# Kernel optimization log

Measured on AMD Instinct MI355X. Metric: run time of the kernel, lower is better.

Reference implementation:

```python
import jax, jax.numpy as jnp
import numpy as np

N = 100000
E = 1600000
G = 64  # number of graphs
EPS = 1e-5
NEG_SLOPE = 0.2


def _gat_conv(x, W, a_src, a_dst, b, src, dst, n, H, C):
    # x: [n, in]; W: [in, H*C]; a_src/a_dst: [H, C]; b: [H*C]
    h = (x @ W).reshape(n, H, C)                      # [n,H,C]
    al_s = jnp.sum(h * a_src, axis=-1)                # [n,H]
    al_d = jnp.sum(h * a_dst, axis=-1)                # [n,H]
    score = jax.nn.leaky_relu(al_s[src] + al_d[dst], NEG_SLOPE)  # [E,H]
    # segment softmax over incoming edges of each dst node
    m = jax.ops.segment_max(score, dst, num_segments=n)
    ex = jnp.exp(score - jax.lax.stop_gradient(m)[dst])
    den = jax.ops.segment_sum(ex, dst, num_segments=n)
    alpha = ex / den[dst]                             # [E,H]
    out = jax.ops.segment_sum(alpha[:, :, None] * h[src], dst, num_segments=n)
    return out.reshape(n, H * C) + b


def _bn_relu(x, gamma, beta):
    mu = jnp.mean(x, axis=0)
    var = jnp.var(x, axis=0)  # biased, matches torch BN normalization
    return jax.nn.relu((x - mu) * jax.lax.rsqrt(var + EPS) * gamma + beta)


def setup_inputs() -> dict:
    key = jax.random.key(0)
    ks = jax.random.split(key, 32)
    d = {}
    d['x'] = jax.random.normal(ks[0], (N, 3), dtype=jnp.float32)
    d['edge_index'] = jax.random.randint(ks[1], (2, E), 0, N, dtype=jnp.int64)
    d['batch'] = jnp.sort(jax.random.randint(ks[2], (N,), 0, G, dtype=jnp.int64))
    def p(k, shape):
        return jax.random.normal(k, shape, dtype=jnp.float32) * 0.1
    # conv1: 3 -> 16, heads=2
    d['W1'] = p(ks[3], (3, 32)); d['as1'] = p(ks[4], (2, 16)); d['ad1'] = p(ks[5], (2, 16)); d['b1'] = p(ks[6], (32,))
    d['g1'] = jnp.ones((32,), jnp.float32); d['be1'] = jnp.zeros((32,), jnp.float32)
    # conv2: 32 -> 32, heads=2
    d['W2'] = p(ks[7], (32, 64)); d['as2'] = p(ks[8], (2, 32)); d['ad2'] = p(ks[9], (2, 32)); d['b2'] = p(ks[10], (64,))
    d['g2'] = jnp.ones((64,), jnp.float32); d['be2'] = jnp.zeros((64,), jnp.float32)
    # conv3: 64 -> 64, heads=2
    d['W3'] = p(ks[11], (64, 128)); d['as3'] = p(ks[12], (2, 64)); d['ad3'] = p(ks[13], (2, 64)); d['b3'] = p(ks[14], (128,))
    d['g3'] = jnp.ones((128,), jnp.float32); d['be3'] = jnp.zeros((128,), jnp.float32)
    d['fcw'] = p(ks[15], (128, 10)); d['fcb'] = p(ks[16], (10,))
    return d


def reference(x, edge_index, batch, W1, as1, ad1, b1, g1, be1, W2, as2, ad2, b2, g2, be2, W3, as3, ad3, b3, g3, be3, fcw, fcb):
    n = x.shape[0]
    loops = jnp.arange(n, dtype=edge_index.dtype)  # PyG GATConv add_self_loops=True
    src = jnp.concatenate([edge_index[0], loops])
    dst = jnp.concatenate([edge_index[1], loops])
    h = _bn_relu(_gat_conv(x, W1, as1, ad1, b1, src, dst, n, 2, 16), g1, be1)
    h = _bn_relu(_gat_conv(h, W2, as2, ad2, b2, src, dst, n, 2, 32), g2, be2)
    h = _bn_relu(_gat_conv(h, W3, as3, ad3, b3, src, dst, n, 2, 64), g3, be3)
    pooled = jax.ops.segment_max(h, batch, num_segments=G)  # [G,128]
    return pooled @ fcw + fcb
```

## Files before the change

### kernel.cpp

```cpp
#include <hip/hip_runtime.h>
#include <cstddef>

constexpr int NN = 100000;
constexpr int NE = 1600000;
constexpr int TE = NE + NN;
constexpr int NG = 64;
constexpr float EPS = 1e-5f;
constexpr float NEG_SLOPE = 0.2f;
constexpr int NREP = 16;

constexpr int NBUCK = 256;
constexpr int DPB = 391;
constexpr int PHB = 256;
constexpr int CH = (TE + PHB - 1) / PHB;

__device__ __forceinline__ unsigned short f2bf(float f) {
    unsigned u = __float_as_uint(f);
    u += 0x7fffu + ((u >> 16) & 1u);
    return (unsigned short)(u >> 16);
}
__device__ __forceinline__ float bf2f(unsigned short s) {
    return __uint_as_float((unsigned)s << 16);
}
__device__ __forceinline__ float bflo(unsigned u) { return __uint_as_float(u << 16); }
__device__ __forceinline__ float bfhi(unsigned u) { return __uint_as_float(u & 0xffff0000u); }


__global__ void k_hist(const int* __restrict__ ei, int* __restrict__ hist) {
    __shared__ int hcnt[NBUCK];
    for (int i = threadIdx.x; i < NBUCK; i += 256) hcnt[i] = 0;
    __syncthreads();
    int k = blockIdx.x;
    int e0 = k * CH, e1 = min(e0 + CH, TE);
    for (int e = e0 + threadIdx.x; e < e1; e += 256) {
        int d = (e < NE) ? ei[NE + e] : (e - NE);
        atomicAdd(&hcnt[d / DPB], 1);
    }
    __syncthreads();
    for (int b = threadIdx.x; b < NBUCK; b += 256) hist[b * PHB + k] = hcnt[b];
}

__global__ void k_scanA(int* __restrict__ hist, int* __restrict__ bsum) {
    __shared__ int ls[PHB];
    int b = blockIdx.x, t = threadIdx.x;
    int v = hist[b * PHB + t];
    ls[t] = v;
    __syncthreads();
    for (int off = 1; off < PHB; off <<= 1) {
        int add = (t >= off) ? ls[t - off] : 0;
        __syncthreads();
        ls[t] += add;
        __syncthreads();
    }
    hist[b * PHB + t] = ls[t] - v;
    if (t == PHB - 1) bsum[b] = ls[t];
}

__global__ void k_scanB(const int* __restrict__ bsum, int* __restrict__ bbase,
                        int* __restrict__ rowptr) {
    __shared__ int ls[NBUCK];
    int t = threadIdx.x;
    int v = bsum[t];
    ls[t] = v;
    __syncthreads();
    for (int off = 1; off < NBUCK; off <<= 1) {
        int add = (t >= off) ? ls[t - off] : 0;
        __syncthreads();
        ls[t] += add;
        __syncthreads();
    }
    bbase[t] = ls[t] - v;
    if (t == NBUCK - 1) { bbase[NBUCK] = ls[t]; rowptr[NN] = ls[t]; }
}

__global__ void k_scatter(const int* __restrict__ ei, const int* __restrict__ hist,
                          const int* __restrict__ bbase, int* __restrict__ pairs) {
    __shared__ int cur[NBUCK];
    int k = blockIdx.x;
    for (int b = threadIdx.x; b < NBUCK; b += 256) cur[b] = bbase[b] + hist[b * PHB + k];
    __syncthreads();
    int e0 = k * CH, e1 = min(e0 + CH, TE);
    for (int e = e0 + threadIdx.x; e < e1; e += 256) {
        int s, d;
        if (e < NE) { s = ei[e]; d = ei[NE + e]; } else { s = e - NE; d = s; }
        int b = d / DPB, ld = d - b * DPB;
        int pos = atomicAdd(&cur[b], 1);
        pairs[pos] = (s << 9) | ld;
    }
}

__global__ void k_csr(const int* __restrict__ pairs, const int* __restrict__ bbase,
                      int* __restrict__ rowptr, int* __restrict__ colsrc) {
    __shared__ int deg[DPB];
    __shared__ int exc[DPB];
    __shared__ int sc[512];
    int b = blockIdx.x, t = threadIdx.x;
    int base = bbase[b], cnt = bbase[b + 1] - base;
    int d0 = b * DPB;
    int ndst = min(DPB, NN - d0);
    for (int i = t; i < DPB; i += 256) deg[i] = 0;
    __syncthreads();
    for (int i = t; i < cnt; i += 256) atomicAdd(&deg[pairs[base + i] & 511], 1);
    __syncthreads();
    sc[t] = (t < DPB) ? deg[t] : 0;
    sc[t + 256] = (t + 256 < DPB) ? deg[t + 256] : 0;
    __syncthreads();
    for (int off = 1; off < 512; off <<= 1) {
        int a0 = (t >= off) ? sc[t - off] : 0;
        int a1 = (t + 256 >= off) ? sc[t + 256 - off] : 0;
        __syncthreads();
        sc[t] += a0; sc[t + 256] += a1;
        __syncthreads();
    }
    if (t < DPB) exc[t] = sc[t] - deg[t];
    if (t + 256 < DPB) exc[t + 256] = sc[t + 256] - deg[t + 256];
    __syncthreads();
    for (int i = t; i < ndst; i += 256) rowptr[d0 + i] = base + exc[i];
    for (int i = t; i < DPB; i += 256) deg[i] = 0;
    __syncthreads();
    for (int i = t; i < cnt; i += 256) {
        int p = pairs[base + i];
        int ld = p & 511;
        int s = (unsigned)p >> 9;
        int pos = base + exc[ld] + atomicAdd(&deg[ld], 1);
        colsrc[pos] = s;
    }
}


template <int IN, int OUT, bool BN, int GRP>
__global__ void k_transform(const void* __restrict__ xv, const float* __restrict__ W,
                            const float* __restrict__ a_src, const float* __restrict__ a_dst,
                            const float* __restrict__ bnrep,
                            const float* __restrict__ gamma, const float* __restrict__ beta,
                            unsigned short* __restrict__ h, float* __restrict__ als,
                            float* __restrict__ ald, int n) {
    constexpr int C = OUT / 2;
    constexpr int TPN = OUT / 4;
    constexpr int NB = 256 / TPN;
    __shared__ float4 Ws4[IN * TPN];
    __shared__ float xs[NB * IN];
    __shared__ float sbn[BN ? 2 * IN : 1];

    if constexpr (BN) {
        if (threadIdx.x < IN) {
            int c = threadIdx.x;
            float s = 0.f, ss = 0.f;
#pragma unroll
            for (int r = 0; r < NREP; ++r) {
                s  += bnrep[r * 2 * IN + c];
                ss += bnrep[r * 2 * IN + IN + c];
            }
            float mu = s / n;
            float var = ss / n - mu * mu;
            float sca = gamma[c] * rsqrtf(var + EPS);
            sbn[c] = sca;
            sbn[IN + c] = beta[c] - mu * sca;
        }
    }
    float* Wsf = (float*)Ws4;
    for (int i = threadIdx.x; i < IN * OUT; i += 256) Wsf[i] = W[i];
    __syncthreads();

    int nl = threadIdx.x / TPN, q = threadIdx.x % TPN;
    int hd = (q >= TPN / 2);
    int cc = (q - hd * (TPN / 2)) * 4;
    float4 as4 = *(const float4*)&a_src[hd * C + cc];
    float4 ad4 = *(const float4*)&a_dst[hd * C + cc];

    for (int g = 0; g < GRP; ++g) {
        int node0 = (blockIdx.x * GRP + g) * NB;
        if (node0 >= n) break;
        if constexpr (BN) {
            const unsigned* xu = (const unsigned*)xv + (size_t)node0 * IN / 2;
            for (int i = threadIdx.x; i < NB * IN / 2; i += 256) {
                int e0 = 2 * i;
                int nn = node0 + e0 / IN;
                unsigned u = (nn < n) ? xu[i] : 0u;
                int c0 = e0 % IN;
                float v0 = bflo(u) * sbn[c0] + sbn[IN + c0];
                float v1 = bfhi(u) * sbn[c0 + 1] + sbn[IN + c0 + 1];
                xs[e0]     = v0 > 0.f ? v0 : 0.f;
                xs[e0 + 1] = v1 > 0.f ? v1 : 0.f;
            }
        } else {
            const float* x = (const float*)xv;
            for (int i = threadIdx.x; i < NB * IN; i += 256) {
                int nn = node0 + i / IN;
                xs[i] = (nn < n) ? x[(size_t)nn * IN + (i % IN)] : 0.f;
            }
        }
        __syncthreads();
        int node = node0 + nl;
        float4 acc = {0.f, 0.f, 0.f, 0.f};
#pragma unroll
        for (int i = 0; i < IN; ++i) {
            float xv2 = xs[nl * IN + i];
            float4 w = Ws4[i * TPN + q];
            acc.x += xv2 * w.x; acc.y += xv2 * w.y; acc.z += xv2 * w.z; acc.w += xv2 * w.w;
        }
        if (node < n) {
            uint2 pk;
            pk.x = (unsigned)f2bf(acc.x) | ((unsigned)f2bf(acc.y) << 16);
            pk.y = (unsigned)f2bf(acc.z) | ((unsigned)f2bf(acc.w) << 16);
            *(uint2*)&h[(size_t)node * OUT + q * 4] = pk;
        }
        float ps = acc.x * as4.x + acc.y * as4.y + acc.z * as4.z + acc.w * as4.w;
        float pd = acc.x * ad4.x + acc.y * ad4.y + acc.z * ad4.z + acc.w * ad4.w;
#pragma unroll
        for (int m = 1; m < TPN / 2; m <<= 1) {
            ps += __shfl_xor(ps, m, 64);
            pd += __shfl_xor(pd, m, 64);
        }
        if ((q & (TPN / 2 - 1)) == 0 && node < n) {
            als[node * 2 + hd] = ps;
            ald[node * 2 + hd] = pd;
        }
        __syncthreads();
    }
}


__device__ __forceinline__ float lrelu(float v) { return v > 0.f ? v : NEG_SLOPE * v; }

template <int OUT>
__global__ void k_aggregate(const int* __restrict__ rowptr, const int* __restrict__ colsrc,
                            const unsigned short* __restrict__ h, const float* __restrict__ als,
                            const float* __restrict__ ald, unsigned short* __restrict__ out,
                            float* __restrict__ bnrep) {
    constexpr int LPE = OUT / 8;
    constexpr int EPI2 = 32 / LPE;
    constexpr int UNR = 4;
    __shared__ float rowbuf[8][OUT];
    __shared__ float4 etab[4][64];
    int wv = threadIdx.x >> 6;
    int lane = threadIdx.x & 63;
    int hw = lane >> 5, hl = lane & 31;
    int base = ((int)blockIdx.x * 4 + wv) * 2;
    int wid = base + hw;
    bool valid = wid < NN;

    int start = 0, cnt = 0;
    float2 dv = make_float2(0.f, 0.f);
    if (valid) {
        start = rowptr[wid];
        cnt = rowptr[wid + 1] - start;
        dv = ((const float2*)ald)[wid];
    }
    int mc = max(cnt, __shfl_xor(cnt, 32, 64));

    if (mc <= 32) {
        int e = start + hl;
        bool act = valid && (hl < cnt);
        int s = act ? colsrc[e] : 0;
        float2 av = act ? ((const float2*)als)[s] : make_float2(0.f, 0.f);
        float t0 = act ? lrelu(av.x + dv.x) : -1e30f;
        float t1 = act ? lrelu(av.y + dv.y) : -1e30f;
        float m0 = t0, m1 = t1;
#pragma unroll
        for (int off = 16; off; off >>= 1) {
            m0 = fmaxf(m0, __shfl_xor(m0, off, 32));
            m1 = fmaxf(m1, __shfl_xor(m1, off, 32));
        }
        float w0 = act ? __expf(t0 - m0) : 0.f;
        float w1 = act ? __expf(t1 - m1) : 0.f;
        float den0 = w0, den1 = w1;
#pragma unroll
        for (int off = 16; off; off >>= 1) {
            den0 += __shfl_xor(den0, off, 32);
            den1 += __shfl_xor(den1, off, 32);
        }
        etab[wv][lane] = make_float4(__int_as_float(s), w0, w1, 0.f);
        int sub = hl / LPE, cl = hl % LPE;
        bool head1 = (cl >= LPE / 2);
        float acc[8];
#pragma unroll
        for (int k = 0; k < 8; ++k) acc[k] = 0.f;
        if (valid) {
            int cm1 = cnt - 1;
            for (int j0 = 0; j0 < cnt; j0 += EPI2 * UNR) {
                float wsl[UNR];
                uint4 hv[UNR];
#pragma unroll
                for (int u = 0; u < UNR; ++u) {
                    int jj = j0 + u * EPI2 + sub;
                    int jc = min(jj, cm1);
                    float4 ed = etab[wv][hw * 32 + jc];
                    wsl[u] = (jj <= cm1) ? (head1 ? ed.z : ed.y) : 0.f;
                    hv[u] = *(const uint4*)&h[(size_t)__float_as_int(ed.x) * OUT + cl * 8];
                }
#pragma unroll
                for (int u = 0; u < UNR; ++u) {
                    float a = wsl[u];
                    acc[0] += a * bflo(hv[u].x); acc[1] += a * bfhi(hv[u].x);
                    acc[2] += a * bflo(hv[u].y); acc[3] += a * bfhi(hv[u].y);
                    acc[4] += a * bflo(hv[u].z); acc[5] += a * bfhi(hv[u].z);
                    acc[6] += a * bflo(hv[u].w); acc[7] += a * bfhi(hv[u].w);
                }
            }
        }
#pragma unroll
        for (int m = LPE; m < 32; m <<= 1) {
#pragma unroll
            for (int k = 0; k < 8; ++k) acc[k] += __shfl_xor(acc[k], m, 32);
        }
        float inv = 1.f / (head1 ? den1 : den0);
        if (valid && sub == 0) {
            float o[8];
#pragma unroll
            for (int k = 0; k < 8; ++k) o[k] = acc[k] * inv;
            uint4 pk;
            pk.x = (unsigned)f2bf(o[0]) | ((unsigned)f2bf(o[1]) << 16);
            pk.y = (unsigned)f2bf(o[2]) | ((unsigned)f2bf(o[3]) << 16);
            pk.z = (unsigned)f2bf(o[4]) | ((unsigned)f2bf(o[5]) << 16);
            pk.w = (unsigned)f2bf(o[6]) | ((unsigned)f2bf(o[7]) << 16);
            *(uint4*)&out[(size_t)wid * OUT + cl * 8] = pk;
            *(float4*)&rowbuf[wv * 2 + hw][cl * 8] = make_float4(o[0], o[1], o[2], o[3]);
            *(float4*)&rowbuf[wv * 2 + hw][cl * 8 + 4] = make_float4(o[4], o[5], o[6], o[7]);
        } else if (!valid) {
            for (int c = hl; c < OUT; c += 32) rowbuf[wv * 2 + hw][c] = 0.f;
        }
    } else {
        for (int i = 0; i < 2; ++i) {
            int w2 = base + i;
            int rb = wv * 2 + i;
            if (w2 >= NN) {
                for (int c = lane; c < OUT; c += 64) rowbuf[rb][c] = 0.f;
                continue;
            }
            int st = rowptr[w2], en = rowptr[w2 + 1];
            float2 dv2 = ((const float2*)ald)[w2];
            constexpr int C = OUT / 2;
            float m0 = -1e30f, m1 = -1e30f;
            for (int e = st + lane; e < en; e += 64) {
                int s = colsrc[e];
                float t0 = lrelu(als[s * 2 + 0] + dv2.x);
                float t1 = lrelu(als[s * 2 + 1] + dv2.y);
                m0 = fmaxf(m0, t0); m1 = fmaxf(m1, t1);
            }
#pragma unroll
            for (int off = 32; off; off >>= 1) {
                m0 = fmaxf(m0, __shfl_xor(m0, off, 64));
                m1 = fmaxf(m1, __shfl_xor(m1, off, 64));
            }
            float den0 = 0.f, den1 = 0.f;
            for (int e = st + lane; e < en; e += 64) {
                int s = colsrc[e];
                float t0 = lrelu(als[s * 2 + 0] + dv2.x);
                float t1 = lrelu(als[s * 2 + 1] + dv2.y);
                den0 += __expf(t0 - m0); den1 += __expf(t1 - m1);
            }
#pragma unroll
            for (int off = 32; off; off >>= 1) {
                den0 += __shfl_xor(den0, off, 64);
                den1 += __shfl_xor(den1, off, 64);
            }
            float inv0 = 1.f / den0, inv1 = 1.f / den1;
            if constexpr (OUT == 128) {
                float a0 = 0.f, a1 = 0.f;
                for (int e = st; e < en; ++e) {
                    int s = colsrc[e];
                    float t0 = lrelu(als[s * 2 + 0] + dv2.x);
                    float t1 = lrelu(als[s * 2 + 1] + dv2.y);
                    float w0 = __expf(t0 - m0) * inv0;
                    float w1 = __expf(t1 - m1) * inv1;
                    a0 += w0 * bf2f(h[(size_t)s * OUT + lane]);
                    a1 += w1 * bf2f(h[(size_t)s * OUT + 64 + lane]);
                }
                out[(size_t)w2 * OUT + lane] = f2bf(a0);
                out[(size_t)w2 * OUT + 64 + lane] = f2bf(a1);
                rowbuf[rb][lane] = a0;
                rowbuf[rb][64 + lane] = a1;
            } else {
                int c = lane;
                bool act2 = c < OUT;
                float a0 = 0.f;
                for (int e = st; e < en; ++e) {
                    int s = colsrc[e];
                    float t0 = lrelu(als[s * 2 + 0] + dv2.x);
                    float t1 = lrelu(als[s * 2 + 1] + dv2.y);
                    float w = (c < C) ? __expf(t0 - m0) * inv0 : __expf(t1 - m1) * inv1;
                    if (act2) a0 += w * bf2f(h[(size_t)s * OUT + c]);
                }
                if (act2) { out[(size_t)w2 * OUT + c] = f2bf(a0); rowbuf[rb][c] = a0; }
            }
        }
    }
    __syncthreads();
    float* dst = &bnrep[(blockIdx.x & (NREP - 1)) * 2 * OUT];
    for (int c = threadIdx.x; c < OUT; c += 256) {
        float s = 0.f, ss = 0.f;
#pragma unroll
        for (int r = 0; r < 8; ++r) {
            float v = rowbuf[r][c];
            s += v; ss += v * v;
        }
        atomicAdd(&dst[c], s);
        atomicAdd(&dst[OUT + c], ss);
    }
}


__global__ void k_pool(const unsigned short* __restrict__ h, const int* __restrict__ batch,
                       const float* __restrict__ bnrep, const float* __restrict__ gamma,
                       const float* __restrict__ beta, float* __restrict__ pooled, int n) {
    const int K = 32;
    int c = threadIdx.x;
    float s = 0.f, ss = 0.f;
#pragma unroll
    for (int r = 0; r < NREP; ++r) {
        s  += bnrep[r * 256 + c];
        ss += bnrep[r * 256 + 128 + c];
    }
    float mu = s / n;
    float var = ss / n - mu * mu;
    float scale = gamma[c] * rsqrtf(var + EPS);
    float shift = beta[c] - mu * scale;
    int n0 = blockIdx.x * K;
    if (n0 >= n) return;
    int nend = min(n, n0 + K);
    int curg = batch[n0];
    float m = 0.f;
    for (int nn = n0; nn < nend; ++nn) {
        int g = batch[nn];
        if (g != curg) {
            atomicMax((int*)&pooled[curg * 128 + c], __float_as_int(m));
            m = 0.f; curg = g;
        }
        float v = bf2f(h[(size_t)nn * 128 + c]) * scale + shift;
        m = fmaxf(m, v > 0.f ? v : 0.f);
    }
    atomicMax((int*)&pooled[curg * 128 + c], __float_as_int(m));
}

__global__ void k_fc(const float* __restrict__ pooled, const float* __restrict__ fcw,
                     const float* __restrict__ fcb, float* __restrict__ out) {
    int t = threadIdx.x;
    if (t >= NG * 10) return;
    int g = t / 10, j = t % 10;
    float acc = fcb[j];
#pragma unroll
    for (int c = 0; c < 128; ++c) acc += pooled[g * 128 + c] * fcw[c * 10 + j];
    out[g * 10 + j] = acc;
}


extern "C" void kernel_launch(void* const* d_in, const int* in_sizes, int n_in,
                              void* d_out, int out_size, void* d_ws, size_t ws_size,
                              hipStream_t stream) {
    const float* x   = (const float*)d_in[0];
    const int*   ei  = (const int*)d_in[1];
    const int*   bat = (const int*)d_in[2];
    const float* W1  = (const float*)d_in[3];
    const float* as1 = (const float*)d_in[4];
    const float* ad1 = (const float*)d_in[5];
    const float* g1  = (const float*)d_in[7];
    const float* be1 = (const float*)d_in[8];
    const float* W2  = (const float*)d_in[9];
    const float* as2 = (const float*)d_in[10];
    const float* ad2 = (const float*)d_in[11];
    const float* g2  = (const float*)d_in[13];
    const float* be2 = (const float*)d_in[14];
    const float* W3  = (const float*)d_in[15];
    const float* as3 = (const float*)d_in[16];
    const float* ad3 = (const float*)d_in[17];
    const float* g3  = (const float*)d_in[19];
    const float* be3 = (const float*)d_in[20];
    const float* fcw = (const float*)d_in[21];
    const float* fcb = (const float*)d_in[22];
    float* out = (float*)d_out;

    char* w = (char*)d_ws;
    size_t off = 0;
    auto take = [&](size_t bytes) {
        void* p = w + off;
        off += (bytes + 255) & ~(size_t)255;
        return p;
    };
    constexpr size_t ZN = (size_t)NREP * 2 * (32 + 64 + 128) + NG * 128;
    char* zreg = (char*)take(ZN * 4);
    float* bnr1   = (float*)zreg;
    float* bnr2   = bnr1 + NREP * 64;
    float* bnr3   = bnr2 + NREP * 128;
    float* pooled = bnr3 + NREP * 256;

    int*   hist    = (int*)take((size_t)NBUCK * PHB * 4);
    int*   bsum    = (int*)take(NBUCK * 4);
    int*   bbase   = (int*)take((NBUCK + 1) * 4);
    int*   rowptr  = (int*)take((size_t)(NN + 1) * 4);
    int*   pairs   = (int*)take((size_t)TE * 4);
    int*   colsrc  = (int*)take((size_t)TE * 4);
    float* al_s    = (float*)take((size_t)NN * 2 * 4);
    float* al_d    = (float*)take((size_t)NN * 2 * 4);
    unsigned short* h0 = (unsigned short*)take((size_t)NN * 128 * 2);
    unsigned short* h1 = (unsigned short*)take((size_t)NN * 128 * 2);

    hipMemsetAsync(zreg, 0, ZN * 4, stream);

    k_hist<<<PHB, 256, 0, stream>>>(ei, hist);
    k_scanA<<<NBUCK, PHB, 0, stream>>>(hist, bsum);
    k_scanB<<<1, NBUCK, 0, stream>>>(bsum, bbase, rowptr);
    k_scatter<<<PHB, 256, 0, stream>>>(ei, hist, bbase, pairs);
    k_csr<<<NBUCK, 256, 0, stream>>>(pairs, bbase, rowptr, colsrc);

    const int AGG_BLOCKS = (NN + 7) / 8;

    k_transform<3, 32, false, 1><<<(NN + 31) / 32, 256, 0, stream>>>(
        x, W1, as1, ad1, nullptr, nullptr, nullptr, h0, al_s, al_d, NN);
    k_aggregate<32><<<AGG_BLOCKS, 256, 0, stream>>>(rowptr, colsrc, h0, al_s, al_d, h1, bnr1);

    k_transform<32, 64, true, 4><<<(NN + 63) / 64, 256, 0, stream>>>(
        h1, W2, as2, ad2, bnr1, g1, be1, h0, al_s, al_d, NN);
    k_aggregate<64><<<AGG_BLOCKS, 256, 0, stream>>>(rowptr, colsrc, h0, al_s, al_d, h1, bnr2);

    k_transform<64, 128, true, 4><<<(NN + 31) / 32, 256, 0, stream>>>(
        h1, W3, as3, ad3, bnr2, g2, be2, h0, al_s, al_d, NN);
    k_aggregate<128><<<AGG_BLOCKS, 256, 0, stream>>>(rowptr, colsrc, h0, al_s, al_d, h1, bnr3);

    k_pool<<<(NN + 31) / 32, 128, 0, stream>>>(h1, bat, bnr3, g3, be3, pooled, NN);
    k_fc<<<1, 640, 0, stream>>>(pooled, fcw, fcb, out);
}
```

Baseline: 358.7 us.

## Aggregate raw inputs before linear transform and fold attention vectors into weights

Reorders each GAT layer as aggregate-then-transform: attention logits come from x·(W·a), precomputed per layer, and the softmax-weighted sum gathers the narrower input features per head. The dense transform is then applied to the per-head aggregates, and BN statistics are gathered in the transform kernel. This shrinks gather width per edge (3/32/64 instead of 32/64/128), cutting the memory traffic of the edge-bound aggregation. In exchange it adds a logits kernel per layer, doubles the accumulators in aggregation (two heads), and requires BN+ReLU to be recomputed on every gathered neighbor.

```diff
diff --git a/kernel.cpp b/kernel.cpp
--- a/kernel.cpp
+++ b/kernel.cpp
@@ -24,6 +24,19 @@
 }
 __device__ __forceinline__ float bflo(unsigned u) { return __uint_as_float(u << 16); }
 __device__ __forceinline__ float bfhi(unsigned u) { return __uint_as_float(u & 0xffff0000u); }
+__device__ __forceinline__ void unpack8(uint4 v, float* f) {
+    f[0] = bflo(v.x); f[1] = bfhi(v.x); f[2] = bflo(v.y); f[3] = bfhi(v.y);
+    f[4] = bflo(v.z); f[5] = bfhi(v.z); f[6] = bflo(v.w); f[7] = bfhi(v.w);
+}
+__device__ __forceinline__ uint4 pack8(const float* o) {
+    uint4 pk;
+    pk.x = (unsigned)f2bf(o[0]) | ((unsigned)f2bf(o[1]) << 16);
+    pk.y = (unsigned)f2bf(o[2]) | ((unsigned)f2bf(o[3]) << 16);
+    pk.z = (unsigned)f2bf(o[4]) | ((unsigned)f2bf(o[5]) << 16);
+    pk.w = (unsigned)f2bf(o[6]) | ((unsigned)f2bf(o[7]) << 16);
+    return pk;
+}
+__device__ __forceinline__ float lrelu(float v) { return v > 0.f ? v : NEG_SLOPE * v; }
 
 
 __global__ void k_hist(const int* __restrict__ ei, int* __restrict__ hist) {
@@ -128,20 +141,127 @@
 }
 
 
-template <int IN, int OUT, bool BN, int GRP>
-__global__ void k_transform(const void* __restrict__ xv, const float* __restrict__ W,
-                            const float* __restrict__ a_src, const float* __restrict__ a_dst,
-                            const float* __restrict__ bnrep,
-                            const float* __restrict__ gamma, const float* __restrict__ beta,
-                            unsigned short* __restrict__ h, float* __restrict__ als,
-                            float* __restrict__ ald, int n) {
-    constexpr int C = OUT / 2;
-    constexpr int TPN = OUT / 4;
-    constexpr int NB = 256 / TPN;
-    __shared__ float4 Ws4[IN * TPN];
-    __shared__ float xs[NB * IN];
+__global__ void k_wa(const float* __restrict__ W1, const float* __restrict__ as1,
+                     const float* __restrict__ ad1,
+                     const float* __restrict__ W2, const float* __restrict__ as2,
+                     const float* __restrict__ ad2,
+                     const float* __restrict__ W3, const float* __restrict__ as3,
+                     const float* __restrict__ ad3,
+                     float* __restrict__ was1, float* __restrict__ wad1,
+                     float* __restrict__ was2, float* __restrict__ wad2,
+                     float* __restrict__ was3, float* __restrict__ wad3) {
+    int t = threadIdx.x;
+    if (t < 6) {
+        int h = t / 3, i = t % 3;
+        float s = 0.f, d = 0.f;
+        for (int c = 0; c < 16; ++c) {
+            float w = W1[i * 32 + h * 16 + c];
+            s += w * as1[h * 16 + c];
+            d += w * ad1[h * 16 + c];
+        }
+        was1[t] = s; wad1[t] = d;
+    }
+    if (t < 64) {
+        int h = t / 32, i = t % 32;
+        float s = 0.f, d = 0.f;
+        for (int c = 0; c < 32; ++c) {
+            float w = W2[i * 64 + h * 32 + c];
+            s += w * as2[h * 32 + c];
+            d += w * ad2[h * 32 + c];
+        }
+        was2[t] = s; wad2[t] = d;
+    }
+    if (t < 128) {
+        int h = t / 64, i = t % 64;
+        float s = 0.f, d = 0.f;
+        for (int c = 0; c < 64; ++c) {
+            float w = W3[i * 128 + h * 64 + c];
+            s += w * as3[h * 64 + c];
+            d += w * ad3[h * 64 + c];
+        }
+        was3[t] = s; wad3[t] = d;
+    }
+}
+
+
+__global__ void k_logits1(const float* __restrict__ x, const float* __restrict__ was,
+                          const float* __restrict__ wad, float* __restrict__ als,
+                          float* __restrict__ ald) {
+    int n = blockIdx.x * 256 + threadIdx.x;
+    if (n >= NN) return;
+    float x0 = x[n * 3], x1 = x[n * 3 + 1], x2 = x[n * 3 + 2];
+    als[n * 2 + 0] = x0 * was[0] + x1 * was[1] + x2 * was[2];
+    als[n * 2 + 1] = x0 * was[3] + x1 * was[4] + x2 * was[5];
+    ald[n * 2 + 0] = x0 * wad[0] + x1 * wad[1] + x2 * wad[2];
+    ald[n * 2 + 1] = x0 * wad[3] + x1 * wad[4] + x2 * wad[5];
+}
+
+template <int IN>
+__global__ void k_logits(const unsigned short* __restrict__ x,
+                         const float* __restrict__ bnrep,
+                         const float* __restrict__ gamma, const float* __restrict__ beta,
+                         const float* __restrict__ was, const float* __restrict__ wad,
+                         float* __restrict__ als, float* __restrict__ ald) {
+    constexpr int P = IN / 8;
+    __shared__ float sbn[2 * IN];
+    __shared__ float swa[4 * IN];
+    if (threadIdx.x < IN) {
+        int c = threadIdx.x;
+        float s = 0.f, ss = 0.f;
+#pragma unroll
+        for (int r = 0; r < NREP; ++r) {
+            s  += bnrep[r * 2 * IN + c];
+            ss += bnrep[r * 2 * IN + IN + c];
+        }
+        float mu = s / NN;
+        float var = ss / NN - mu * mu;
+        float sca = gamma[c] * rsqrtf(var + EPS);
+        sbn[c] = sca;
+        sbn[IN + c] = beta[c] - mu * sca;
+    }
+    for (int i = threadIdx.x; i < 2 * IN; i += 256) {
+        swa[i] = was[i];
+        swa[2 * IN + i] = wad[i];
+    }
+    __syncthreads();
+    int idx = blockIdx.x * 256 + threadIdx.x;
+    int node = idx / P, pl = idx % P;
+    if (node >= NN) return;
+    uint4 v = *(const uint4*)&x[(size_t)node * IN + pl * 8];
+    float f[8];
+    unpack8(v, f);
+    float s0 = 0.f, s1 = 0.f, d0 = 0.f, d1 = 0.f;
+#pragma unroll
+    for (int k = 0; k < 8; ++k) {
+        int c = pl * 8 + k;
+        float t = f[k] * sbn[c] + sbn[IN + c];
+        t = t > 0.f ? t : 0.f;
+        s0 += t * swa[c];           s1 += t * swa[IN + c];
+        d0 += t * swa[2 * IN + c];  d1 += t * swa[3 * IN + c];
+    }
+#pragma unroll
+    for (int m = 1; m < P; m <<= 1) {
+        s0 += __shfl_xor(s0, m, 64); s1 += __shfl_xor(s1, m, 64);
+        d0 += __shfl_xor(d0, m, 64); d1 += __shfl_xor(d1, m, 64);
+    }
+    if (pl == 0) {
+        als[node * 2 + 0] = s0; als[node * 2 + 1] = s1;
+        ald[node * 2 + 0] = d0; ald[node * 2 + 1] = d1;
+    }
+}
+
+
+template <int IN, bool BN>
+__global__ void k_agg(const int* __restrict__ rowptr, const int* __restrict__ colsrc,
+                      const unsigned short* __restrict__ x,
+                      const float* __restrict__ als, const float* __restrict__ ald,
+                      const float* __restrict__ bnrep, const float* __restrict__ gamma,
+                      const float* __restrict__ beta, unsigned short* __restrict__ agg) {
+    constexpr int LPE = IN / 8;
+    constexpr int EPI2 = 32 / LPE;
+    constexpr int UNR = 2;
+    __shared__ float4 etab[4][64];
     __shared__ float sbn[BN ? 2 * IN : 1];
-
     if constexpr (BN) {
         if (threadIdx.x < IN) {
             int c = threadIdx.x;
@@ -151,95 +271,19 @@
                 s  += bnrep[r * 2 * IN + c];
                 ss += bnrep[r * 2 * IN + IN + c];
             }
-            float mu = s / n;
-            float var = ss / n - mu * mu;
+            float mu = s / NN;
+            float var = ss / NN - mu * mu;
             float sca = gamma[c] * rsqrtf(var + EPS);
             sbn[c] = sca;
             sbn[IN + c] = beta[c] - mu * sca;
         }
-    }
-    float* Wsf = (float*)Ws4;
-    for (int i = threadIdx.x; i < IN * OUT; i += 256) Wsf[i] = W[i];
-    __syncthreads();
-
-    int nl = threadIdx.x / TPN, q = threadIdx.x % TPN;
-    int hd = (q >= TPN / 2);
-    int cc = (q - hd * (TPN / 2)) * 4;
-    float4 as4 = *(const float4*)&a_src[hd * C + cc];
-    float4 ad4 = *(const float4*)&a_dst[hd * C + cc];
-
-    for (int g = 0; g < GRP; ++g) {
-        int node0 = (blockIdx.x * GRP + g) * NB;
-        if (node0 >= n) break;
-        if constexpr (BN) {
-            const unsigned* xu = (const unsigned*)xv + (size_t)node0 * IN / 2;
-            for (int i = threadIdx.x; i < NB * IN / 2; i += 256) {
-                int e0 = 2 * i;
-                int nn = node0 + e0 / IN;
-                unsigned u = (nn < n) ? xu[i] : 0u;
-                int c0 = e0 % IN;
-                float v0 = bflo(u) * sbn[c0] + sbn[IN + c0];
-                float v1 = bfhi(u) * sbn[c0 + 1] + sbn[IN + c0 + 1];
-                xs[e0]     = v0 > 0.f ? v0 : 0.f;
-                xs[e0 + 1] = v1 > 0.f ? v1 : 0.f;
-            }
-        } else {
-            const float* x = (const float*)xv;
-            for (int i = threadIdx.x; i < NB * IN; i += 256) {
-                int nn = node0 + i / IN;
-                xs[i] = (nn < n) ? x[(size_t)nn * IN + (i % IN)] : 0.f;
-            }
-        }
-        __syncthreads();
-        int node = node0 + nl;
-        float4 acc = {0.f, 0.f, 0.f, 0.f};
-#pragma unroll
-        for (int i = 0; i < IN; ++i) {
-            float xv2 = xs[nl * IN + i];
-            float4 w = Ws4[i * TPN + q];
-            acc.x += xv2 * w.x; acc.y += xv2 * w.y; acc.z += xv2 * w.z; acc.w += xv2 * w.w;
-        }
-        if (node < n) {
-            uint2 pk;
-            pk.x = (unsigned)f2bf(acc.x) | ((unsigned)f2bf(acc.y) << 16);
-            pk.y = (unsigned)f2bf(acc.z) | ((unsigned)f2bf(acc.w) << 16);
-            *(uint2*)&h[(size_t)node * OUT + q * 4] = pk;
-        }
-        float ps = acc.x * as4.x + acc.y * as4.y + acc.z * as4.z + acc.w * as4.w;
-        float pd = acc.x * ad4.x + acc.y * ad4.y + acc.z * ad4.z + acc.w * ad4.w;
-#pragma unroll
-        for (int m = 1; m < TPN / 2; m <<= 1) {
-            ps += __shfl_xor(ps, m, 64);
-            pd += __shfl_xor(pd, m, 64);
-        }
-        if ((q & (TPN / 2 - 1)) == 0 && node < n) {
-            als[node * 2 + hd] = ps;
-            ald[node * 2 + hd] = pd;
-        }
-        __syncthreads();
-    }
-}
-
-
-__device__ __forceinline__ float lrelu(float v) { return v > 0.f ? v : NEG_SLOPE * v; }
-
-template <int OUT>
-__global__ void k_aggregate(const int* __restrict__ rowptr, const int* __restrict__ colsrc,
-                            const unsigned short* __restrict__ h, const float* __restrict__ als,
-                            const float* __restrict__ ald, unsigned short* __restrict__ out,
-                            float* __restrict__ bnrep) {
-    constexpr int LPE = OUT / 8;
-    constexpr int EPI2 = 32 / LPE;
-    constexpr int UNR = 4;
-    __shared__ float rowbuf[8][OUT];
-    __shared__ float4 etab[4][64];
-    int wv = threadIdx.x >> 6;
-    int lane = threadIdx.x & 63;
+        __syncthreads();
+    }
+    int wv = threadIdx.x >> 6, lane = threadIdx.x & 63;
     int hw = lane >> 5, hl = lane & 31;
     int base = ((int)blockIdx.x * 4 + wv) * 2;
     int wid = base + hw;
     bool valid = wid < NN;
-
     int start = 0, cnt = 0;
     float2 dv = make_float2(0.f, 0.f);
     if (valid) {
@@ -270,73 +314,70 @@
             den0 += __shfl_xor(den0, off, 32);
             den1 += __shfl_xor(den1, off, 32);
         }
-        etab[wv][lane] = make_float4(__int_as_float(s), w0, w1, 0.f);
+        float i0 = valid ? 1.f / den0 : 0.f;
+        float i1 = valid ? 1.f / den1 : 0.f;
+        etab[wv][lane] = make_float4(__int_as_float(s), w0 * i0, w1 * i1, 0.f);
         int sub = hl / LPE, cl = hl % LPE;
-        bool head1 = (cl >= LPE / 2);
-        float acc[8];
-#pragma unroll
-        for (int k = 0; k < 8; ++k) acc[k] = 0.f;
+        float bsc[8], bsh[8];
+        if constexpr (BN) {
+#pragma unroll
+            for (int k = 0; k < 8; ++k) { bsc[k] = sbn[cl * 8 + k]; bsh[k] = sbn[IN + cl * 8 + k]; }
+        }
+        float a0[8], a1[8];
+#pragma unroll
+        for (int k = 0; k < 8; ++k) { a0[k] = 0.f; a1[k] = 0.f; }
         if (valid) {
             int cm1 = cnt - 1;
             for (int j0 = 0; j0 < cnt; j0 += EPI2 * UNR) {
-                float wsl[UNR];
+                float l0[UNR], l1[UNR];
                 uint4 hv[UNR];
 #pragma unroll
                 for (int u = 0; u < UNR; ++u) {
                     int jj = j0 + u * EPI2 + sub;
                     int jc = min(jj, cm1);
                     float4 ed = etab[wv][hw * 32 + jc];
-                    wsl[u] = (jj <= cm1) ? (head1 ? ed.z : ed.y) : 0.f;
-                    hv[u] = *(const uint4*)&h[(size_t)__float_as_int(ed.x) * OUT + cl * 8];
+                    bool on = jj <= cm1;
+                    l0[u] = on ? ed.y : 0.f;
+                    l1[u] = on ? ed.z : 0.f;
+                    hv[u] = *(const uint4*)&x[(size_t)__float_as_int(ed.x) * IN + cl * 8];
                 }
 #pragma unroll
                 for (int u = 0; u < UNR; ++u) {
-                    float a = wsl[u];
-                    acc[0] += a * bflo(hv[u].x); acc[1] += a * bfhi(hv[u].x);
-                    acc[2] += a * bflo(hv[u].y); acc[3] += a * bfhi(hv[u].y);
-                    acc[4] += a * bflo(hv[u].z); acc[5] += a * bfhi(hv[u].z);
-                    acc[6] += a * bflo(hv[u].w); acc[7] += a * bfhi(hv[u].w);
+                    float f[8];
+                    unpack8(hv[u], f);
+#pragma unroll
+                    for (int k = 0; k < 8; ++k) {
+                        float vv = f[k];
+                        if constexpr (BN) { vv = vv * bsc[k] + bsh[k]; vv = vv > 0.f ? vv : 0.f; }
+                        a0[k] += l0[u] * vv;
+                        a1[k] += l1[u] * vv;
+                    }
                 }
             }
         }
 #pragma unroll
         for (int m = LPE; m < 32; m <<= 1) {
 #pragma unroll
-            for (int k = 0; k < 8; ++k) acc[k] += __shfl_xor(acc[k], m, 32);
-        }
-        float inv = 1.f / (head1 ? den1 : den0);
+            for (int k = 0; k < 8; ++k) {
+                a0[k] += __shfl_xor(a0[k], m, 64);
+                a1[k] += __shfl_xor(a1[k], m, 64);
+            }
+        }
         if (valid && sub == 0) {
-            float o[8];
-#pragma unroll
-            for (int k = 0; k < 8; ++k) o[k] = acc[k] * inv;
-            uint4 pk;
-            pk.x = (unsigned)f2bf(o[0]) | ((unsigned)f2bf(o[1]) << 16);
-            pk.y = (unsigned)f2bf(o[2]) | ((unsigned)f2bf(o[3]) << 16);
-            pk.z = (unsigned)f2bf(o[4]) | ((unsigned)f2bf(o[5]) << 16);
-            pk.w = (unsigned)f2bf(o[6]) | ((unsigned)f2bf(o[7]) << 16);
-            *(uint4*)&out[(size_t)wid * OUT + cl * 8] = pk;
-            *(float4*)&rowbuf[wv * 2 + hw][cl * 8] = make_float4(o[0], o[1], o[2], o[3]);
-            *(float4*)&rowbuf[wv * 2 + hw][cl * 8 + 4] = make_float4(o[4], o[5], o[6], o[7]);
-        } else if (!valid) {
-            for (int c = hl; c < OUT; c += 32) rowbuf[wv * 2 + hw][c] = 0.f;
+            *(uint4*)&agg[(size_t)wid * 2 * IN + cl * 8] = pack8(a0);
+            *(uint4*)&agg[(size_t)wid * 2 * IN + IN + cl * 8] = pack8(a1);
         }
     } else {
-        for (int i = 0; i < 2; ++i) {
-            int w2 = base + i;
-            int rb = wv * 2 + i;
-            if (w2 >= NN) {
-                for (int c = lane; c < OUT; c += 64) rowbuf[rb][c] = 0.f;
-                continue;
-            }
+        for (int i2 = 0; i2 < 2; ++i2) {
+            int w2 = base + i2;
+            if (w2 >= NN) continue;
             int st = rowptr[w2], en = rowptr[w2 + 1];
             float2 dv2 = ((const float2*)ald)[w2];
-            constexpr int C = OUT / 2;
             float m0 = -1e30f, m1 = -1e30f;
             for (int e = st + lane; e < en; e += 64) {
                 int s = colsrc[e];
-                float t0 = lrelu(als[s * 2 + 0] + dv2.x);
-                float t1 = lrelu(als[s * 2 + 1] + dv2.y);
-                m0 = fmaxf(m0, t0); m1 = fmaxf(m1, t1);
+                m0 = fmaxf(m0, lrelu(als[s * 2 + 0] + dv2.x));
+                m1 = fmaxf(m1, lrelu(als[s * 2 + 1] + dv2.y));
             }
 #pragma unroll
             for (int off = 32; off; off >>= 1) {
@@ -346,9 +387,8 @@
             float den0 = 0.f, den1 = 0.f;
             for (int e = st + lane; e < en; e += 64) {
                 int s = colsrc[e];
-                float t0 = lrelu(als[s * 2 + 0] + dv2.x);
-                float t1 = lrelu(als[s * 2 + 1] + dv2.y);
-                den0 += __expf(t0 - m0); den1 += __expf(t1 - m1);
+                den0 += __expf(lrelu(als[s * 2 + 0] + dv2.x) - m0);
+                den1 += __expf(lrelu(als[s * 2 + 1] + dv2.y) - m1);
             }
 #pragma unroll
             for (int off = 32; off; off >>= 1) {
@@ -356,48 +396,236 @@
                 den1 += __shfl_xor(den1, off, 64);
             }
             float inv0 = 1.f / den0, inv1 = 1.f / den1;
-            if constexpr (OUT == 128) {
-                float a0 = 0.f, a1 = 0.f;
-                for (int e = st; e < en; ++e) {
-                    int s = colsrc[e];
-                    float t0 = lrelu(als[s * 2 + 0] + dv2.x);
-                    float t1 = lrelu(als[s * 2 + 1] + dv2.y);
-                    float w0 = __expf(t0 - m0) * inv0;
-                    float w1 = __expf(t1 - m1) * inv1;
-                    a0 += w0 * bf2f(h[(size_t)s * OUT + lane]);
-                    a1 += w1 * bf2f(h[(size_t)s * OUT + 64 + lane]);
+            int c = lane;
+            float sc_ = 1.f, sh_ = 0.f;
+            if constexpr (BN) {
+                if (c < IN) { sc_ = sbn[c]; sh_ = sbn[IN + c]; }
+            }
+            float a0 = 0.f, a1 = 0.f;
+            for (int e = st; e < en; ++e) {
+                int s = colsrc[e];
+                float aa0 = __expf(lrelu(als[s * 2 + 0] + dv2.x) - m0) * inv0;
+                float aa1 = __expf(lrelu(als[s * 2 + 1] + dv2.y) - m1) * inv1;
+                if (c < IN) {
+                    float vv = bf2f(x[(size_t)s * IN + c]);
+                    if constexpr (BN) { vv = vv * sc_ + sh_; vv = vv > 0.f ? vv : 0.f; }
+                    a0 += aa0 * vv;
+                    a1 += aa1 * vv;
                 }
-                out[(size_t)w2 * OUT + lane] = f2bf(a0);
-                out[(size_t)w2 * OUT + 64 + lane] = f2bf(a1);
-                rowbuf[rb][lane] = a0;
-                rowbuf[rb][64 + lane] = a1;
-            } else {
-                int c = lane;
-                bool act2 = c < OUT;
-                float a0 = 0.f;
-                for (int e = st; e < en; ++e) {
-                    int s = colsrc[e];
-                    float t0 = lrelu(als[s * 2 + 0] + dv2.x);
-                    float t1 = lrelu(als[s * 2 + 1] + dv2.y);
-                    float w = (c < C) ? __expf(t0 - m0) * inv0 : __expf(t1 - m1) * inv1;
-                    if (act2) a0 += w * bf2f(h[(size_t)s * OUT + c]);
-                }
-                if (act2) { out[(size_t)w2 * OUT + c] = f2bf(a0); rowbuf[rb][c] = a0; }
-            }
-        }
+            }
+            if (c < IN) {
+                agg[(size_t)w2 * 2 * IN + c] = f2bf(a0);
+                agg[(size_t)w2 * 2 * IN + IN + c] = f2bf(a1);
+            }
+        }
+    }
+}
+
+__global__ void k_agg1(const int* __restrict__ rowptr, const int* __restrict__ colsrc,
+                       const float* __restrict__ x, const float* __restrict__ als,
+                       const float* __restrict__ ald, float* __restrict__ agg) {
+    int wv = threadIdx.x >> 6, lane = threadIdx.x & 63;
+    int hw = lane >> 5, hl = lane & 31;
+    int base = ((int)blockIdx.x * 4 + wv) * 2;
+    int wid = base + hw;
+    bool valid = wid < NN;
+    int start = 0, cnt = 0;
+    float2 dv = make_float2(0.f, 0.f);
+    if (valid) {
+        start = rowptr[wid];
+        cnt = rowptr[wid + 1] - start;
+        dv = ((const float2*)ald)[wid];
+    }
+    int mc = max(cnt, __shfl_xor(cnt, 32, 64));
+    if (mc <= 32) {
+        int e = start + hl;
+        bool act = valid && (hl < cnt);
+        int s = act ? colsrc[e] : 0;
+        float2 av = act ? ((const float2*)als)[s] : make_float2(0.f, 0.f);
+        float t0 = act ? lrelu(av.x + dv.x) : -1e30f;
+        float t1 = act ? lrelu(av.y + dv.y) : -1e30f;
+        float m0 = t0, m1 = t1;
+#pragma unroll
+        for (int off = 16; off; off >>= 1) {
+            m0 = fmaxf(m0, __shfl_xor(m0, off, 32));
+            m1 = fmaxf(m1, __shfl_xor(m1, off, 32));
+        }
+        float w0 = act ? __expf(t0 - m0) : 0.f;
+        float w1 = act ? __expf(t1 - m1) : 0.f;
+        float den0 = w0, den1 = w1;
+#pragma unroll
+        for (int off = 16; off; off >>= 1) {
+            den0 += __shfl_xor(den0, off, 32);
+            den1 += __shfl_xor(den1, off, 32);
+        }
+        float a[6];
+#pragma unroll
+        for (int k = 0; k < 6; ++k) a[k] = 0.f;
+        if (act) {
+            float al0 = w0 / den0, al1 = w1 / den1;
+            float x0 = x[s * 3], x1 = x[s * 3 + 1], x2 = x[s * 3 + 2];
+            a[0] = al0 * x0; a[1] = al0 * x1; a[2] = al0 * x2;
+            a[3] = al1 * x0; a[4] = al1 * x1; a[5] = al1 * x2;
+        }
+#pragma unroll
+        for (int m = 1; m < 32; m <<= 1) {
+#pragma unroll
+            for (int k = 0; k < 6; ++k) a[k] += __shfl_xor(a[k], m, 64);
+        }
+        if (valid && hl == 0) {
+#pragma unroll
+            for (int k = 0; k < 6; ++k) agg[(size_t)wid * 6 + k] = a[k];
+        }
+    } else {
+        for (int i2 = 0; i2 < 2; ++i2) {
+            int w2 = base + i2;
+            if (w2 >= NN) continue;
+            int st = rowptr[w2], en = rowptr[w2 + 1];
+            float2 dv2 = ((const float2*)ald)[w2];
+            float m0 = -1e30f, m1 = -1e30f;
+            for (int e = st + lane; e < en; e += 64) {
+                int s = colsrc[e];
+                m0 = fmaxf(m0, lrelu(als[s * 2 + 0] + dv2.x));
+                m1 = fmaxf(m1, lrelu(als[s * 2 + 1] + dv2.y));
+            }
+#pragma unroll
+            for (int off = 32; off; off >>= 1) {
+                m0 = fmaxf(m0, __shfl_xor(m0, off, 64));
+                m1 = fmaxf(m1, __shfl_xor(m1, off, 64));
+            }
+            float den0 = 0.f, den1 = 0.f;
+            for (int e = st + lane; e < en; e += 64) {
+                int s = colsrc[e];
+                den0 += __expf(lrelu(als[s * 2 + 0] + dv2.x) - m0);
+                den1 += __expf(lrelu(als[s * 2 + 1] + dv2.y) - m1);
+            }
+#pragma unroll
+            for (int off = 32; off; off >>= 1) {
+                den0 += __shfl_xor(den0, off, 64);
+                den1 += __shfl_xor(den1, off, 64);
+            }
+            float inv0 = 1.f / den0, inv1 = 1.f / den1;
+            float a[6];
+#pragma unroll
+            for (int k = 0; k < 6; ++k) a[k] = 0.f;
+            for (int e = st + lane; e < en; e += 64) {
+                int s = colsrc[e];
+                float aa0 = __expf(lrelu(als[s * 2 + 0] + dv2.x) - m0) * inv0;
+                float aa1 = __expf(lrelu(als[s * 2 + 1] + dv2.y) - m1) * inv1;
+                float x0 = x[s * 3], x1 = x[s * 3 + 1], x2 = x[s * 3 + 2];
+                a[0] += aa0 * x0; a[1] += aa0 * x1; a[2] += aa0 * x2;
+                a[3] += aa1 * x0; a[4] += aa1 * x1; a[5] += aa1 * x2;
+            }
+#pragma unroll
+            for (int m = 1; m < 64; m <<= 1) {
+#pragma unroll
+                for (int k = 0; k < 6; ++k) a[k] += __shfl_xor(a[k], m, 64);
+            }
+            if (lane == 0) {
+#pragma unroll
+                for (int k = 0; k < 6; ++k) agg[(size_t)w2 * 6 + k] = a[k];
+            }
+        }
+    }
+}
+
+
+template <int IN, int OUT, int GRP>
+__global__ void k_transform(const unsigned short* __restrict__ agg,
+                            const float* __restrict__ W,
+                            unsigned short* __restrict__ xout,
+                            float* __restrict__ bnrep, int n) {
+    constexpr int TPN = OUT / 4;
+    constexpr int NB = 256 / TPN;
+    __shared__ float4 Ws4[IN * TPN];
+    __shared__ float xs[NB * 2 * IN];
+    __shared__ float red[2 * OUT];
+    float* Wsf = (float*)Ws4;
+    for (int i = threadIdx.x; i < IN * OUT; i += 256) Wsf[i] = W[i];
+    for (int i = threadIdx.x; i < 2 * OUT; i += 256) red[i] = 0.f;
+    __syncthreads();
+    int nl = threadIdx.x / TPN, q = threadIdx.x % TPN;
+    int hd = (q >= TPN / 2);
+    float s4[4] = {0.f, 0.f, 0.f, 0.f}, ss4[4] = {0.f, 0.f, 0.f, 0.f};
+    for (int g = 0; g < GRP; ++g) {
+        int node0 = (blockIdx.x * GRP + g) * NB;
+        if (node0 >= n) break;
+        const unsigned* au = (const unsigned*)agg + (size_t)node0 * IN;
+        for (int i = threadIdx.x; i < NB * IN; i += 256) {
+            int nn = node0 + i / IN;
+            unsigned u = (nn < n) ? au[i] : 0u;
+            xs[2 * i] = bflo(u);
+            xs[2 * i + 1] = bfhi(u);
+        }
+        __syncthreads();
+        int node = node0 + nl;
+        float4 acc = {0.f, 0.f, 0.f, 0.f};
+#pragma unroll
+        for (int i = 0; i < IN; ++i) {
+            float xv = xs[nl * 2 * IN + hd * IN + i];
+            float4 w = Ws4[i * TPN + q];
+            acc.x += xv * w.x; acc.y += xv * w.y; acc.z += xv * w.z; acc.w += xv * w.w;
+        }
+        if (node < n) {
+            uint2 pk;
+            pk.x = (unsigned)f2bf(acc.x) | ((unsigned)f2bf(acc.y) << 16);
+            pk.y = (unsigned)f2bf(acc.z) | ((unsigned)f2bf(acc.w) << 16);
+            *(uint2*)&xout[(size_t)node * OUT + q * 4] = pk;
+            s4[0] += acc.x; s4[1] += acc.y; s4[2] += acc.z; s4[3] += acc.w;
+            ss4[0] += acc.x * acc.x; ss4[1] += acc.y * acc.y;
+            ss4[2] += acc.z * acc.z; ss4[3] += acc.w * acc.w;
+        }
+        __syncthreads();
+    }
+#pragma unroll
+    for (int k = 0; k < 4; ++k) {
+        atomicAdd(&red[q * 4 + k], s4[k]);
+        atomicAdd(&red[OUT + q * 4 + k], ss4[k]);
     }
     __syncthreads();
     float* dst = &bnrep[(blockIdx.x & (NREP - 1)) * 2 * OUT];
-    for (int c = threadIdx.x; c < OUT; c += 256) {
-        float s = 0.f, ss = 0.f;
-#pragma unroll
-        for (int r = 0; r < 8; ++r) {
-            float v = rowbuf[r][c];
-            s += v; ss += v * v;
-        }
-        atomicAdd(&dst[c], s);
-        atomicAdd(&dst[OUT + c], ss);
-    }
+    for (int i = threadIdx.x; i < 2 * OUT; i += 256) atomicAdd(&dst[i], red[i]);
+}
+
+__global__ void k_transform1(const float* __restrict__ agg, const float* __restrict__ W,
+                             unsigned short* __restrict__ xout, float* __restrict__ bnrep,
+                             int n) {
+    __shared__ float Wsf[3 * 32];
+    __shared__ float xs[32 * 6];
+    __shared__ float red[64];
+    for (int i = threadIdx.x; i < 96; i += 256) Wsf[i] = W[i];
+    for (int i = threadIdx.x; i < 64; i += 256) red[i] = 0.f;
+    int node0 = blockIdx.x * 32;
+    for (int i = threadIdx.x; i < 192; i += 256) {
+        int nn = node0 + i / 6;
+        xs[i] = (nn < n) ? agg[(size_t)node0 * 6 + i] : 0.f;
+    }
+    __syncthreads();
+    int nl = threadIdx.x / 8, q = threadIdx.x % 8;
+    int hd = (q >= 4);
+    int node = node0 + nl;
+    float4 acc = {0.f, 0.f, 0.f, 0.f};
+#pragma unroll
+    for (int i = 0; i < 3; ++i) {
+        float xv = xs[nl * 6 + hd * 3 + i];
+        acc.x += xv * Wsf[i * 32 + q * 4 + 0];
+        acc.y += xv * Wsf[i * 32 + q * 4 + 1];
+        acc.z += xv * Wsf[i * 32 + q * 4 + 2];
+        acc.w += xv * Wsf[i * 32 + q * 4 + 3];
+    }
+    if (node < n) {
+        uint2 pk;
+        pk.x = (unsigned)f2bf(acc.x) | ((unsigned)f2bf(acc.y) << 16);
+        pk.y = (unsigned)f2bf(acc.z) | ((unsigned)f2bf(acc.w) << 16);
+        *(uint2*)&xout[(size_t)node * 32 + q * 4] = pk;
+        atomicAdd(&red[q * 4 + 0], acc.x); atomicAdd(&red[32 + q * 4 + 0], acc.x * acc.x);
+        atomicAdd(&red[q * 4 + 1], acc.y); atomicAdd(&red[32 + q * 4 + 1], acc.y * acc.y);
+        atomicAdd(&red[q * 4 + 2], acc.z); atomicAdd(&red[32 + q * 4 + 2], acc.z * acc.z);
+        atomicAdd(&red[q * 4 + 3], acc.w); atomicAdd(&red[32 + q * 4 + 3], acc.w * acc.w);
+    }
+    __syncthreads();
+    float* dst = &bnrep[(blockIdx.x & (NREP - 1)) * 64];
+    for (int i = threadIdx.x; i < 64; i += 256) atomicAdd(&dst[i], red[i]);
 }
 
 
@@ -492,8 +720,17 @@
     int*   colsrc  = (int*)take((size_t)TE * 4);
     float* al_s    = (float*)take((size_t)NN * 2 * 4);
     float* al_d    = (float*)take((size_t)NN * 2 * 4);
-    unsigned short* h0 = (unsigned short*)take((size_t)NN * 128 * 2);
-    unsigned short* h1 = (unsigned short*)take((size_t)NN * 128 * 2);
+    float* was1    = (float*)take(64);
+    float* wad1    = (float*)take(64);
+    float* was2    = (float*)take(64 * 4);
+    float* wad2    = (float*)take(64 * 4);
+    float* was3    = (float*)take(128 * 4);
+    float* wad3    = (float*)take(128 * 4);
+    float* agg1f   = (float*)take((size_t)NN * 6 * 4);
+    unsigned short* aggb = (unsigned short*)take((size_t)NN * 128 * 2);
+    unsigned short* x2 = (unsigned short*)take((size_t)NN * 32 * 2);
+    unsigned short* x3 = (unsigned short*)take((size_t)NN * 64 * 2);
+    unsigned short* x4 = (unsigned short*)take((size_t)NN * 128 * 2);
 
     hipMemsetAsync(zreg, 0, ZN * 4, stream);
 
@@ -503,20 +740,27 @@
     k_scatter<<<PHB, 256, 0, stream>>>(ei, hist, bbase, pairs);
     k_csr<<<NBUCK, 256, 0, stream>>>(pairs, bbase, rowptr, colsrc);
 
+    k_wa<<<1, 256, 0, stream>>>(W1, as1, ad1, W2, as2, ad2, W3, as3, ad3,
+                                was1, wad1, was2, wad2, was3, wad3);
+
     const int AGG_BLOCKS = (NN + 7) / 8;
 
-    k_transform<3, 32, false, 1><<<(NN + 31) / 32, 256, 0, stream>>>(
-        x, W1, as1, ad1, nullptr, nullptr, nullptr, h0, al_s, al_d, NN);
-    k_aggregate<32><<<AGG_BLOCKS, 256, 0, stream>>>(rowptr, colsrc, h0, al_s, al_d, h1, bnr1);
-
-    k_transform<32, 64, true, 4><<<(NN + 63) / 64, 256, 0, stream>>>(
-        h1, W2, as2, ad2, bnr1, g1, be1, h0, al_s, al_d, NN);
-    k_aggregate<64><<<AGG_BLOCKS, 256, 0, stream>>>(rowptr, colsrc, h0, al_s, al_d, h1, bnr2);
-
-    k_transform<64, 128, true, 4><<<(NN + 31) / 32, 256, 0, stream>>>(
-        h1, W3, as3, ad3, bnr2, g2, be2, h0, al_s, al_d, NN);
-    k_aggregate<128><<<AGG_BLOCKS, 256, 0, stream>>>(rowptr, colsrc, h0, al_s, al_d, h1, bnr3);
-
-    k_pool<<<(NN + 31) / 32, 128, 0, stream>>>(h1, bat, bnr3, g3, be3, pooled, NN);
+    k_logits1<<<(NN + 255) / 256, 256, 0, stream>>>(x, was1, wad1, al_s, al_d);
+    k_agg1<<<AGG_BLOCKS, 256, 0, stream>>>(rowptr, colsrc, x, al_s, al_d, agg1f);
+    k_transform1<<<(NN + 31) / 32, 256, 0, stream>>>(agg1f, W1, x2, bnr1, NN);
+
+    k_logits<32><<<(NN * 4 + 255) / 256, 256, 0, stream>>>(x2, bnr1, g1, be1, was2, wad2,
+                                                           al_s, al_d);
+    k_agg<32, true><<<AGG_BLOCKS, 256, 0, stream>>>(rowptr, colsrc, x2, al_s, al_d,
+                                                    bnr1, g1, be1, aggb);
+    k_transform<32, 64, 4><<<(NN + 63) / 64, 256, 0, stream>>>(aggb, W2, x3, bnr2, NN);
+
+    k_logits<64><<<(NN * 8 + 255) / 256, 256, 0, stream>>>(x3, bnr2, g2, be2, was3, wad3,
+                                                           al_s, al_d);
+    k_agg<64, true><<<AGG_BLOCKS, 256, 0, stream>>>(rowptr, colsrc, x3, al_s, al_d,
+                                                    bnr2, g2, be2, aggb);
+    k_transform<64, 128, 4><<<(NN + 31) / 32, 256, 0, stream>>>(aggb, W3, x4, bnr3, NN);
+
+    k_pool<<<(NN + 31) / 32, 128, 0, stream>>>(x4, bat, bnr3, g3, be3, pooled, NN);
     k_fc<<<1, 640, 0, stream>>>(pooled, fcw, fcb, out);
 }
```

New measurement: 419.6 us. +17.0%, slower.
